# Optimization experiments

Measured on AMD Instinct MI355X. Metric: run time of the kernel, lower is better.

Reference implementation:

```python
import jax, jax.numpy as jnp
import numpy as np

N = 100000   # nodes (single node type 'word')
R = 4        # relation types (sorted rel_names)
E = 160000   # edges per relation
H = 128      # h_dim
O = 64       # out_dim


def setup_inputs() -> dict:
    key = jax.random.key(0)
    k0, k1, k2, k3 = jax.random.split(key, 4)
    embed = jax.random.normal(k0, (N, H), jnp.float32) * 0.1          # RelGraphEmbed table
    weight = jax.random.normal(k1, (R, H, O), jnp.float32) / np.sqrt(H)  # layer-2 per-rel weight
    bias1 = jnp.zeros((H,), jnp.float32)   # layer-1 h_bias
    bias2 = jnp.zeros((O,), jnp.float32)   # layer-2 h_bias
    edge_src = jax.random.randint(k2, (R, E), 0, N)
    edge_dst = jax.random.randint(k3, (R, E), 0, N)
    return dict(embed=embed, weight=weight, bias1=bias1, bias2=bias2,
                edge_src=edge_src, edge_dst=edge_dst)


def _rel_mean(x, src, dst, num_nodes):
    # GraphConv(norm='right'): sum messages into dst, divide by dst in-degree.
    msg = x[src]                                                    # [E, d] gather
    summed = jax.ops.segment_sum(msg, dst, num_segments=num_nodes)  # scatter-add
    deg = jax.ops.segment_sum(jnp.ones(src.shape, x.dtype), dst, num_segments=num_nodes)
    return summed / jnp.maximum(deg, 1.0)[:, None]


def reference(embed, weight, bias1, bias2, edge_src, edge_dst):
    n = embed.shape[0]
    # Layer 1: weight=False -> HeteroGraphConv sums right-normalized aggregations, then bias+relu.
    h1 = jnp.zeros_like(embed)
    for r in range(edge_src.shape[0]):
        h1 = h1 + _rel_mean(embed, edge_src[r], edge_dst[r], n)
    h1 = jax.nn.relu(h1 + bias1)
    # Layer 2: per-relation linear transform, aggregate, sum over relations, bias (no activation).
    out = jnp.zeros((n, weight.shape[-1]), embed.dtype)
    for r in range(edge_src.shape[0]):
        out = out + _rel_mean(h1 @ weight[r], edge_src[r], edge_dst[r], n)
    return out + bias2
```

## Files before the change

### kernel.cpp

```cpp
#include <hip/hip_runtime.h>
#include <hip/hip_bf16.h>

#define H 128
#define O 64
#define RELS 4

typedef short short8 __attribute__((ext_vector_type(8)));
typedef float f32x4 __attribute__((ext_vector_type(4)));

static __device__ __forceinline__ unsigned short f2b(float x) {
    __hip_bfloat16 h = __float2bfloat16(x);
    return *reinterpret_cast<unsigned short*>(&h);
}
static __device__ __forceinline__ float blo(unsigned u) { return __uint_as_float(u << 16); }
static __device__ __forceinline__ float bhi(unsigned u) { return __uint_as_float(u & 0xffff0000u); }

#define ACC8(acc, uv, wt)                                           \
    acc[0] += (wt) * blo(uv.x); acc[1] += (wt) * bhi(uv.x);         \
    acc[2] += (wt) * blo(uv.y); acc[3] += (wt) * bhi(uv.y);         \
    acc[4] += (wt) * blo(uv.z); acc[5] += (wt) * bhi(uv.z);         \
    acc[6] += (wt) * blo(uv.w); acc[7] += (wt) * bhi(uv.w);

__global__ void k_prep(const float* __restrict__ embed, unsigned short* __restrict__ eb,
                       const float* __restrict__ W, unsigned short* __restrict__ WT,
                       const int* __restrict__ dst, int* __restrict__ cnt,
                       int n4, int wtot, int E, int RE, int N, int b_cvt, int b_w) {
    int b = blockIdx.x;
    if (b < b_cvt) {
        int base = b * 1024;
#pragma unroll
        for (int k = 0; k < 4; ++k) {
            int i = base + k * 256 + threadIdx.x;
            if (i < n4) {
                float4 v = ((const float4*)embed)[i];
                ushort4 o;
                o.x = f2b(v.x); o.y = f2b(v.y); o.z = f2b(v.z); o.w = f2b(v.w);
                ((ushort4*)eb)[i] = o;
            }
        }
    } else if (b < b_cvt + b_w) {
        int i = (b - b_cvt) * 256 + threadIdx.x;
        if (i < wtot) {
            int r = i >> 13;
            int n = (i >> 7) & (O - 1);
            int k = i & (H - 1);
            WT[i] = f2b(W[((size_t)r * H + k) * O + n]);
        }
    } else {
        int i = (b - b_cvt - b_w) * 256 + threadIdx.x;
        if (i < RE) { int r = i / E; atomicAdd(&cnt[r * N + dst[i]], 1); }
    }
}

__global__ void k_scan1(const int* __restrict__ cnt, int* __restrict__ offs,
                        int* __restrict__ bsum, int n, int N_) {
    __shared__ int sh[256];
    int t = threadIdx.x;
    int base = blockIdx.x * 1024 + t * 4;
    int4 v = make_int4(0, 0, 0, 0);
    if (base + 3 < n && (N_ & 3) == 0) {
#pragma unroll
        for (int r = 0; r < RELS; ++r) {
            int4 c = *(const int4*)(cnt + (size_t)r * N_ + base);
            v.x += c.x; v.y += c.y; v.z += c.z; v.w += c.w;
        }
    } else {
        for (int j = 0; j < 4; ++j) {
            int i = base + j;
            if (i < n) {
                int s = 0;
                for (int r = 0; r < RELS; ++r) s += cnt[(size_t)r * N_ + i];
                (&v.x)[j] = s;
            }
        }
    }
    int s = v.x + v.y + v.z + v.w;
    sh[t] = s; __syncthreads();
    for (int off = 1; off < 256; off <<= 1) {
        int x = (t >= off) ? sh[t - off] : 0;
        __syncthreads();
        sh[t] += x;
        __syncthreads();
    }
    int incl = sh[t];
    int ex = incl - s;
    if (base < n)     offs[base]     = ex;
    if (base + 1 < n) offs[base + 1] = ex + v.x;
    if (base + 2 < n) offs[base + 2] = ex + v.x + v.y;
    if (base + 3 < n) offs[base + 3] = ex + v.x + v.y + v.z;
    if (t == 255) bsum[blockIdx.x] = incl;
}

__global__ void k_scan2(int* __restrict__ bsum, int nb) {
    __shared__ int sh[512];
    int t = threadIdx.x;
    int s = (t < nb) ? bsum[t] : 0;
    sh[t] = s; __syncthreads();
    for (int off = 1; off < 512; off <<= 1) {
        int x = (t >= off) ? sh[t - off] : 0;
        __syncthreads();
        sh[t] += x;
        __syncthreads();
    }
    if (t < nb) bsum[t] = sh[t] - s;
}

__global__ void k_scan3c(int* __restrict__ offs, const int* __restrict__ bsum,
                         const int* __restrict__ cnt, int* __restrict__ cursor,
                         int n, int total, int N_) {
    int i = blockIdx.x * blockDim.x + threadIdx.x;
    if (i < n) {
        int off = offs[i] + bsum[i >> 10];
        offs[i] = off;
        int c0 = cnt[i], c1 = cnt[N_ + i], c2 = cnt[2 * N_ + i];
        cursor[i]          = off;
        cursor[N_ + i]     = off + c0;
        cursor[2 * N_ + i] = off + c0 + c1;
        cursor[3 * N_ + i] = off + c0 + c1 + c2;
    }
    if (i == 0) offs[n] = total;
}

__global__ void k_fill(const int* __restrict__ src, const int* __restrict__ dst,
                       const int* __restrict__ cnt, int* __restrict__ cursor,
                       uint2* __restrict__ ue, int E, int RE, int N) {
    int i = blockIdx.x * blockDim.x + threadIdx.x;
    if (i >= RE) return;
    int r = i / E;
    int d = dst[i];
    int pos = atomicAdd(&cursor[r * N + d], 1);
    float w = 1.0f / (float)max(cnt[r * N + d], 1);
    ue[pos] = make_uint2((unsigned)(r * N + src[i]), __float_as_uint(w));
}

__global__ void k_pull1(const unsigned short* __restrict__ eb, const int* __restrict__ offs2,
                        const uint2* __restrict__ ue, const float* __restrict__ bias1,
                        unsigned short* __restrict__ h1, int N) {
    int node = blockIdx.x * 16 + (threadIdx.x >> 4);
    if (node >= N) return;
    int q = threadIdx.x & 15;
    int beg = offs2[node], end = offs2[node + 1];
    unsigned N1 = (unsigned)N, N2 = (unsigned)(2 * N);

    float a[8] = {0.f, 0.f, 0.f, 0.f, 0.f, 0.f, 0.f, 0.f};
    float c[8] = {0.f, 0.f, 0.f, 0.f, 0.f, 0.f, 0.f, 0.f};

    int e = beg;
    for (; e + 2 <= end; e += 2) {
        uint2 p0 = ue[e], p1 = ue[e + 1];
        unsigned s0 = p0.x; if (s0 >= N2) s0 -= N2; if (s0 >= N1) s0 -= N1;
        unsigned s1 = p1.x; if (s1 >= N2) s1 -= N2; if (s1 >= N1) s1 -= N1;
        float w0 = __uint_as_float(p0.y), w1 = __uint_as_float(p1.y);
        uint4 u0 = *(const uint4*)(eb + (size_t)s0 * H + q * 8);
        uint4 u1 = *(const uint4*)(eb + (size_t)s1 * H + q * 8);
        ACC8(a, u0, w0);
        ACC8(c, u1, w1);
    }
    if (e < end) {
        uint2 p0 = ue[e];
        unsigned s0 = p0.x; if (s0 >= N2) s0 -= N2; if (s0 >= N1) s0 -= N1;
        float w0 = __uint_as_float(p0.y);
        uint4 u0 = *(const uint4*)(eb + (size_t)s0 * H + q * 8);
        ACC8(a, u0, w0);
    }

    float4 b0 = *(const float4*)(bias1 + q * 8);
    float4 b1 = *(const float4*)(bias1 + q * 8 + 4);
    float f0 = fmaxf(a[0] + c[0] + b0.x, 0.f);
    float f1 = fmaxf(a[1] + c[1] + b0.y, 0.f);
    float f2 = fmaxf(a[2] + c[2] + b0.z, 0.f);
    float f3 = fmaxf(a[3] + c[3] + b0.w, 0.f);
    float f4 = fmaxf(a[4] + c[4] + b1.x, 0.f);
    float f5 = fmaxf(a[5] + c[5] + b1.y, 0.f);
    float f6 = fmaxf(a[6] + c[6] + b1.z, 0.f);
    float f7 = fmaxf(a[7] + c[7] + b1.w, 0.f);
    uint4 o;
    o.x = (unsigned)f2b(f0) | ((unsigned)f2b(f1) << 16);
    o.y = (unsigned)f2b(f2) | ((unsigned)f2b(f3) << 16);
    o.z = (unsigned)f2b(f4) | ((unsigned)f2b(f5) << 16);
    o.w = (unsigned)f2b(f6) | ((unsigned)f2b(f7) << 16);
    *(uint4*)(h1 + (size_t)node * H + q * 8) = o;
}

__global__ __launch_bounds__(256) void k_gemm(const unsigned short* __restrict__ h1,
                                              const unsigned short* __restrict__ WT,
                                              unsigned short* __restrict__ T, int N) {
    __shared__ __align__(16) unsigned short st[4][32][72];
    int tid = threadIdx.x, wv = tid >> 6, l = tid & 63;
    int row0 = blockIdx.x * 32;
    int rA = l & 15, kb = (l >> 4) * 8;

    short8 af[2][4];
#pragma unroll
    for (int mf = 0; mf < 2; ++mf)
#pragma unroll
        for (int kk = 0; kk < 4; ++kk) {
            int row = row0 + mf * 16 + rA;
            short8 v = {0, 0, 0, 0, 0, 0, 0, 0};
            if (row < N) v = *(const short8*)(h1 + (size_t)row * H + kk * 32 + kb);
            af[mf][kk] = v;
        }

    const unsigned short* Wb = WT + (size_t)wv * O * H;
    f32x4 z = {0.f, 0.f, 0.f, 0.f};
    f32x4 acc[2][4];
#pragma unroll
    for (int mf = 0; mf < 2; ++mf)
#pragma unroll
        for (int nt = 0; nt < 4; ++nt) acc[mf][nt] = z;

#pragma unroll
    for (int nt = 0; nt < 4; ++nt) {
        short8 bf[4];
#pragma unroll
        for (int kk = 0; kk < 4; ++kk)
            bf[kk] = *(const short8*)(Wb + ((size_t)(nt * 16 + rA)) * H + kk * 32 + kb);
#pragma unroll
        for (int kk = 0; kk < 4; ++kk)
#pragma unroll
            for (int mf = 0; mf < 2; ++mf)
                acc[mf][nt] = __builtin_amdgcn_mfma_f32_16x16x32_bf16(
                    af[mf][kk], bf[kk], acc[mf][nt], 0, 0, 0);
    }

#pragma unroll
    for (int mf = 0; mf < 2; ++mf)
#pragma unroll
        for (int nt = 0; nt < 4; ++nt)
#pragma unroll
            for (int j = 0; j < 4; ++j)
                st[wv][mf * 16 + (l >> 4) * 4 + j][nt * 16 + rA] = f2b(acc[mf][nt][j]);

#pragma unroll
    for (int i = 0; i < 4; ++i) {
        int rr = i * 8 + (l >> 3);
        uint4 v = *(const uint4*)&st[wv][rr][(l & 7) * 8];
        int grow = row0 + rr;
        if (grow < N)
            *(uint4*)(T + ((size_t)wv * N + grow) * O + (l & 7) * 8) = v;
    }
}

__global__ void k_pull2(const unsigned short* __restrict__ T, const int* __restrict__ offs2,
                        const uint2* __restrict__ ue, const float* __restrict__ bias2,
                        float* __restrict__ out, int N) {
    int node = blockIdx.x * 32 + (threadIdx.x >> 3);
    if (node >= N) return;
    int o = threadIdx.x & 7;
    int beg = offs2[node], end = offs2[node + 1];

    float a[8] = {0.f, 0.f, 0.f, 0.f, 0.f, 0.f, 0.f, 0.f};
    float c[8] = {0.f, 0.f, 0.f, 0.f, 0.f, 0.f, 0.f, 0.f};

    int e = beg;
    for (; e + 2 <= end; e += 2) {
        uint2 p0 = ue[e], p1 = ue[e + 1];
        float w0 = __uint_as_float(p0.y), w1 = __uint_as_float(p1.y);
        uint4 u0 = *(const uint4*)(T + (size_t)p0.x * O + o * 8);
        uint4 u1 = *(const uint4*)(T + (size_t)p1.x * O + o * 8);
        ACC8(a, u0, w0);
        ACC8(c, u1, w1);
    }
    if (e < end) {
        uint2 p0 = ue[e];
        float w0 = __uint_as_float(p0.y);
        uint4 u0 = *(const uint4*)(T + (size_t)p0.x * O + o * 8);
        ACC8(a, u0, w0);
    }

    float4 b0 = *(const float4*)(bias2 + o * 8);
    float4 b1 = *(const float4*)(bias2 + o * 8 + 4);
    float4 v0, v1;
    v0.x = a[0] + c[0] + b0.x; v0.y = a[1] + c[1] + b0.y;
    v0.z = a[2] + c[2] + b0.z; v0.w = a[3] + c[3] + b0.w;
    v1.x = a[4] + c[4] + b1.x; v1.y = a[5] + c[5] + b1.y;
    v1.z = a[6] + c[6] + b1.z; v1.w = a[7] + c[7] + b1.w;
    *(float4*)(out + (size_t)node * O + o * 8)     = v0;
    *(float4*)(out + (size_t)node * O + o * 8 + 4) = v1;
}

extern "C" void kernel_launch(void* const* d_in, const int* in_sizes, int n_in,
                              void* d_out, int out_size, void* d_ws, size_t ws_size,
                              hipStream_t stream) {
    const float* embed  = (const float*)d_in[0];
    const float* weight = (const float*)d_in[1];
    const float* bias1  = (const float*)d_in[2];
    const float* bias2  = (const float*)d_in[3];
    const int*   esrc   = (const int*)d_in[4];
    const int*   edst   = (const int*)d_in[5];
    float* out = (float*)d_out;

    const int N = in_sizes[0] / H;
    const int E = in_sizes[4] / RELS;
    const int RN = RELS * N;
    const int RE = RELS * E;

    char* p = (char*)d_ws;
    auto alloc = [&](size_t bytes) {
        char* q = p;
        p += (bytes + 255) & ~(size_t)255;
        return q;
    };
    int* cnt    = (int*)alloc((size_t)RN * 4);
    int* offs2  = (int*)alloc(((size_t)N + 1) * 4);
    int* cursor = (int*)alloc((size_t)RN * 4);
    int* bsum   = (int*)alloc(4096);
    uint2* ue   = (uint2*)alloc((size_t)RE * 8);
    unsigned short* eb  = (unsigned short*)alloc((size_t)N * H * 2);
    unsigned short* h1  = (unsigned short*)alloc((size_t)N * H * 2);
    unsigned short* WT  = (unsigned short*)alloc((size_t)RELS * O * H * 2);
    unsigned short* T   = (unsigned short*)alloc((size_t)RELS * N * O * 2);

    hipMemsetAsync(cnt, 0, (size_t)RN * 4, stream);

    int n4 = N * H / 4;
    int wtot = RELS * O * H;
    int b_cvt = (n4 + 1023) / 1024;
    int b_w   = (wtot + 255) / 256;
    int b_h   = (RE + 255) / 256;
    k_prep<<<b_cvt + b_w + b_h, 256, 0, stream>>>(embed, eb, weight, WT, edst, cnt,
                                                  n4, wtot, E, RE, N, b_cvt, b_w);

    int nb = (N + 1023) / 1024;
    k_scan1<<<nb, 256, 0, stream>>>(cnt, offs2, bsum, N, N);
    k_scan2<<<1, 512, 0, stream>>>(bsum, nb);
    k_scan3c<<<(N + 255) / 256, 256, 0, stream>>>(offs2, bsum, cnt, cursor, N, RE, N);

    k_fill<<<(RE + 255) / 256, 256, 0, stream>>>(esrc, edst, cnt, cursor, ue, E, RE, N);

    k_pull1<<<(N + 15) / 16, 256, 0, stream>>>(eb, offs2, ue, bias1, h1, N);

    k_gemm<<<(N + 31) / 32, 256, 0, stream>>>(h1, WT, T, N);

    k_pull2<<<(N + 31) / 32, 256, 0, stream>>>(T, offs2, ue, bias2, out, N);
}
```

Baseline: 176.1 us.

## Fuse layer-1 pull aggregation with per-relation GEMM through shared memory

The layer-1 gather/mean/relu kernel and the per-relation MFMA GEMM are merged into one kernel. Each block aggregates 16 nodes into an LDS tile, then runs the 16x128 by 128x64 bf16 GEMM for the four relations, one per wave. This removes the h1 global round trip and one kernel launch. The cost is a smaller GEMM tile per block (16 rows instead of 32), so WT fragments are reloaded twice as often. It also adds a block barrier between the irregular gather phase and the GEMM. The prep kernel is also reordered so the degree-count atomics blocks are scheduled first.

Result: no change. 177.9 us (+1.0%).

```diff
diff --git a/kernel.cpp b/kernel.cpp
--- a/kernel.cpp
+++ b/kernel.cpp
@@ -24,10 +24,13 @@
 __global__ void k_prep(const float* __restrict__ embed, unsigned short* __restrict__ eb,
                        const float* __restrict__ W, unsigned short* __restrict__ WT,
                        const int* __restrict__ dst, int* __restrict__ cnt,
-                       int n4, int wtot, int E, int RE, int N, int b_cvt, int b_w) {
+                       int n4, int wtot, int E, int RE, int N, int b_h, int b_cvt) {
     int b = blockIdx.x;
-    if (b < b_cvt) {
-        int base = b * 1024;
+    if (b < b_h) {
+        int i = b * 256 + threadIdx.x;
+        if (i < RE) { int r = i / E; atomicAdd(&cnt[r * N + dst[i]], 1); }
+    } else if (b < b_h + b_cvt) {
+        int base = (b - b_h) * 1024;
 #pragma unroll
         for (int k = 0; k < 4; ++k) {
             int i = base + k * 256 + threadIdx.x;
@@ -38,17 +41,14 @@
                 ((ushort4*)eb)[i] = o;
             }
         }
-    } else if (b < b_cvt + b_w) {
-        int i = (b - b_cvt) * 256 + threadIdx.x;
+    } else {
+        int i = (b - b_h - b_cvt) * 256 + threadIdx.x;
         if (i < wtot) {
             int r = i >> 13;
             int n = (i >> 7) & (O - 1);
             int k = i & (H - 1);
             WT[i] = f2b(W[((size_t)r * H + k) * O + n]);
         }
-    } else {
-        int i = (b - b_cvt - b_w) * 256 + threadIdx.x;
-        if (i < RE) { int r = i / E; atomicAdd(&cnt[r * N + dst[i]], 1); }
     }
 }
 
@@ -133,82 +133,74 @@
     ue[pos] = make_uint2((unsigned)(r * N + src[i]), __float_as_uint(w));
 }
 
-__global__ void k_pull1(const unsigned short* __restrict__ eb, const int* __restrict__ offs2,
-                        const uint2* __restrict__ ue, const float* __restrict__ bias1,
-                        unsigned short* __restrict__ h1, int N) {
-    int node = blockIdx.x * 16 + (threadIdx.x >> 4);
-    if (node >= N) return;
-    int q = threadIdx.x & 15;
-    int beg = offs2[node], end = offs2[node + 1];
-    unsigned N1 = (unsigned)N, N2 = (unsigned)(2 * N);
+__global__ __launch_bounds__(256) void k_l1g(const unsigned short* __restrict__ eb,
+                                             const int* __restrict__ offs2,
+                                             const uint2* __restrict__ ue,
+                                             const float* __restrict__ bias1,
+                                             const unsigned short* __restrict__ WT,
+                                             unsigned short* __restrict__ T, int N) {
+    __shared__ __align__(16) unsigned short hs[16][136];
+    __shared__ __align__(16) unsigned short st[4][16][72];
+    int tid = threadIdx.x, wv = tid >> 6, l = tid & 63;
+    int row0 = blockIdx.x * 16;
+    int nloc = tid >> 4;
+    int node = row0 + nloc;
+    int q = l & 15;
 
     float a[8] = {0.f, 0.f, 0.f, 0.f, 0.f, 0.f, 0.f, 0.f};
     float c[8] = {0.f, 0.f, 0.f, 0.f, 0.f, 0.f, 0.f, 0.f};
-
-    int e = beg;
-    for (; e + 2 <= end; e += 2) {
-        uint2 p0 = ue[e], p1 = ue[e + 1];
-        unsigned s0 = p0.x; if (s0 >= N2) s0 -= N2; if (s0 >= N1) s0 -= N1;
-        unsigned s1 = p1.x; if (s1 >= N2) s1 -= N2; if (s1 >= N1) s1 -= N1;
-        float w0 = __uint_as_float(p0.y), w1 = __uint_as_float(p1.y);
-        uint4 u0 = *(const uint4*)(eb + (size_t)s0 * H + q * 8);
-        uint4 u1 = *(const uint4*)(eb + (size_t)s1 * H + q * 8);
-        ACC8(a, u0, w0);
-        ACC8(c, u1, w1);
-    }
-    if (e < end) {
-        uint2 p0 = ue[e];
-        unsigned s0 = p0.x; if (s0 >= N2) s0 -= N2; if (s0 >= N1) s0 -= N1;
-        float w0 = __uint_as_float(p0.y);
-        uint4 u0 = *(const uint4*)(eb + (size_t)s0 * H + q * 8);
-        ACC8(a, u0, w0);
-    }
-
-    float4 b0 = *(const float4*)(bias1 + q * 8);
-    float4 b1 = *(const float4*)(bias1 + q * 8 + 4);
-    float f0 = fmaxf(a[0] + c[0] + b0.x, 0.f);
-    float f1 = fmaxf(a[1] + c[1] + b0.y, 0.f);
-    float f2 = fmaxf(a[2] + c[2] + b0.z, 0.f);
-    float f3 = fmaxf(a[3] + c[3] + b0.w, 0.f);
-    float f4 = fmaxf(a[4] + c[4] + b1.x, 0.f);
-    float f5 = fmaxf(a[5] + c[5] + b1.y, 0.f);
-    float f6 = fmaxf(a[6] + c[6] + b1.z, 0.f);
-    float f7 = fmaxf(a[7] + c[7] + b1.w, 0.f);
-    uint4 o;
-    o.x = (unsigned)f2b(f0) | ((unsigned)f2b(f1) << 16);
-    o.y = (unsigned)f2b(f2) | ((unsigned)f2b(f3) << 16);
-    o.z = (unsigned)f2b(f4) | ((unsigned)f2b(f5) << 16);
-    o.w = (unsigned)f2b(f6) | ((unsigned)f2b(f7) << 16);
-    *(uint4*)(h1 + (size_t)node * H + q * 8) = o;
-}
-
-__global__ __launch_bounds__(256) void k_gemm(const unsigned short* __restrict__ h1,
-                                              const unsigned short* __restrict__ WT,
-                                              unsigned short* __restrict__ T, int N) {
-    __shared__ __align__(16) unsigned short st[4][32][72];
-    int tid = threadIdx.x, wv = tid >> 6, l = tid & 63;
-    int row0 = blockIdx.x * 32;
+    if (node < N) {
+        int beg = offs2[node], end = offs2[node + 1];
+        unsigned N1 = (unsigned)N, N2 = (unsigned)(2 * N);
+        int e = beg;
+        for (; e + 2 <= end; e += 2) {
+            uint2 p0 = ue[e], p1 = ue[e + 1];
+            unsigned s0 = p0.x; if (s0 >= N2) s0 -= N2; if (s0 >= N1) s0 -= N1;
+            unsigned s1 = p1.x; if (s1 >= N2) s1 -= N2; if (s1 >= N1) s1 -= N1;
+            float w0 = __uint_as_float(p0.y), w1 = __uint_as_float(p1.y);
+            uint4 u0 = *(const uint4*)(eb + (size_t)s0 * H + q * 8);
+            uint4 u1 = *(const uint4*)(eb + (size_t)s1 * H + q * 8);
+            ACC8(a, u0, w0);
+            ACC8(c, u1, w1);
+        }
+        if (e < end) {
+            uint2 p0 = ue[e];
+            unsigned s0 = p0.x; if (s0 >= N2) s0 -= N2; if (s0 >= N1) s0 -= N1;
+            float w0 = __uint_as_float(p0.y);
+            uint4 u0 = *(const uint4*)(eb + (size_t)s0 * H + q * 8);
+            ACC8(a, u0, w0);
+        }
+        float4 b0 = *(const float4*)(bias1 + q * 8);
+        float4 b1 = *(const float4*)(bias1 + q * 8 + 4);
+        float f0 = fmaxf(a[0] + c[0] + b0.x, 0.f);
+        float f1 = fmaxf(a[1] + c[1] + b0.y, 0.f);
+        float f2 = fmaxf(a[2] + c[2] + b0.z, 0.f);
+        float f3 = fmaxf(a[3] + c[3] + b0.w, 0.f);
+        float f4 = fmaxf(a[4] + c[4] + b1.x, 0.f);
+        float f5 = fmaxf(a[5] + c[5] + b1.y, 0.f);
+        float f6 = fmaxf(a[6] + c[6] + b1.z, 0.f);
+        float f7 = fmaxf(a[7] + c[7] + b1.w, 0.f);
+        uint4 o;
+        o.x = (unsigned)f2b(f0) | ((unsigned)f2b(f1) << 16);
+        o.y = (unsigned)f2b(f2) | ((unsigned)f2b(f3) << 16);
+        o.z = (unsigned)f2b(f4) | ((unsigned)f2b(f5) << 16);
+        o.w = (unsigned)f2b(f6) | ((unsigned)f2b(f7) << 16);
+        *(uint4*)&hs[nloc][q * 8] = o;
+    } else {
+        uint4 zz = make_uint4(0, 0, 0, 0);
+        *(uint4*)&hs[nloc][q * 8] = zz;
+    }
+    __syncthreads();
+
     int rA = l & 15, kb = (l >> 4) * 8;
-
-    short8 af[2][4];
-#pragma unroll
-    for (int mf = 0; mf < 2; ++mf)
-#pragma unroll
-        for (int kk = 0; kk < 4; ++kk) {
-            int row = row0 + mf * 16 + rA;
-            short8 v = {0, 0, 0, 0, 0, 0, 0, 0};
-            if (row < N) v = *(const short8*)(h1 + (size_t)row * H + kk * 32 + kb);
-            af[mf][kk] = v;
-        }
+    short8 af[4];
+#pragma unroll
+    for (int kk = 0; kk < 4; ++kk)
+        af[kk] = *(const short8*)&hs[rA][kk * 32 + kb];
 
     const unsigned short* Wb = WT + (size_t)wv * O * H;
     f32x4 z = {0.f, 0.f, 0.f, 0.f};
-    f32x4 acc[2][4];
-#pragma unroll
-    for (int mf = 0; mf < 2; ++mf)
-#pragma unroll
-        for (int nt = 0; nt < 4; ++nt) acc[mf][nt] = z;
-
+    f32x4 acc[4] = {z, z, z, z};
 #pragma unroll
     for (int nt = 0; nt < 4; ++nt) {
         short8 bf[4];
@@ -217,22 +209,17 @@
             bf[kk] = *(const short8*)(Wb + ((size_t)(nt * 16 + rA)) * H + kk * 32 + kb);
 #pragma unroll
         for (int kk = 0; kk < 4; ++kk)
-#pragma unroll
-            for (int mf = 0; mf < 2; ++mf)
-                acc[mf][nt] = __builtin_amdgcn_mfma_f32_16x16x32_bf16(
-                    af[mf][kk], bf[kk], acc[mf][nt], 0, 0, 0);
-    }
-
-#pragma unroll
-    for (int mf = 0; mf < 2; ++mf)
-#pragma unroll
-        for (int nt = 0; nt < 4; ++nt)
-#pragma unroll
-            for (int j = 0; j < 4; ++j)
-                st[wv][mf * 16 + (l >> 4) * 4 + j][nt * 16 + rA] = f2b(acc[mf][nt][j]);
-
-#pragma unroll
-    for (int i = 0; i < 4; ++i) {
+            acc[nt] = __builtin_amdgcn_mfma_f32_16x16x32_bf16(af[kk], bf[kk], acc[nt], 0, 0, 0);
+    }
+
+#pragma unroll
+    for (int nt = 0; nt < 4; ++nt)
+#pragma unroll
+        for (int j = 0; j < 4; ++j)
+            st[wv][(l >> 4) * 4 + j][nt * 16 + rA] = f2b(acc[nt][j]);
+
+#pragma unroll
+    for (int i = 0; i < 2; ++i) {
         int rr = i * 8 + (l >> 3);
         uint4 v = *(const uint4*)&st[wv][rr][(l & 7) * 8];
         int grow = row0 + rr;
@@ -307,7 +294,6 @@
     int* bsum   = (int*)alloc(4096);
     uint2* ue   = (uint2*)alloc((size_t)RE * 8);
     unsigned short* eb  = (unsigned short*)alloc((size_t)N * H * 2);
-    unsigned short* h1  = (unsigned short*)alloc((size_t)N * H * 2);
     unsigned short* WT  = (unsigned short*)alloc((size_t)RELS * O * H * 2);
     unsigned short* T   = (unsigned short*)alloc((size_t)RELS * N * O * 2);
 
@@ -315,11 +301,11 @@
 
     int n4 = N * H / 4;
     int wtot = RELS * O * H;
+    int b_h   = (RE + 255) / 256;
     int b_cvt = (n4 + 1023) / 1024;
     int b_w   = (wtot + 255) / 256;
-    int b_h   = (RE + 255) / 256;
-    k_prep<<<b_cvt + b_w + b_h, 256, 0, stream>>>(embed, eb, weight, WT, edst, cnt,
-                                                  n4, wtot, E, RE, N, b_cvt, b_w);
+    k_prep<<<b_h + b_cvt + b_w, 256, 0, stream>>>(embed, eb, weight, WT, edst, cnt,
+                                                  n4, wtot, E, RE, N, b_h, b_cvt);
 
     int nb = (N + 1023) / 1024;
     k_scan1<<<nb, 256, 0, stream>>>(cnt, offs2, bsum, N, N);
@@ -328,9 +314,7 @@
 
     k_fill<<<(RE + 255) / 256, 256, 0, stream>>>(esrc, edst, cnt, cursor, ue, E, RE, N);
 
-    k_pull1<<<(N + 15) / 16, 256, 0, stream>>>(eb, offs2, ue, bias1, h1, N);
-
-    k_gemm<<<(N + 31) / 32, 256, 0, stream>>>(h1, WT, T, N);
+    k_l1g<<<(N + 15) / 16, 256, 0, stream>>>(eb, offs2, ue, bias1, WT, T, N);
 
     k_pull2<<<(N + 31) / 32, 256, 0, stream>>>(T, offs2, ue, bias2, out, N);
 }
```
